# Kernel tuning notes

Hardware: AMD Instinct MI355X
Metric: run time of the kernel (lower is better)

The kernel has to match this reference:

```python
import jax, jax.numpy as jnp
import numpy as np

B, L, D, FF = 4, 4096, 1024, 4096
EPS = 1e-06


def setup_inputs() -> dict:
    key = jax.random.key(0)
    ks = jax.random.split(key, 20)
    s_d = 1.0 / np.sqrt(D)
    s_ff = 1.0 / np.sqrt(FF)
    inp = {
        "x": jax.random.normal(ks[0], (B, L, D), jnp.float32),
        "hidden": jax.random.normal(ks[1], (B, D), jnp.float32),
        # sioconv linears (stored as [in, out])
        "w_ln_z": jax.random.normal(ks[2], (D, D), jnp.float32) * s_d,
        "b_ln_z": jnp.zeros((D,), jnp.float32),
        "w_dt": jax.random.normal(ks[3], (D, D), jnp.float32) * s_d,
        "b_dt": jnp.zeros((D,), jnp.float32),
        "w_y": jax.random.normal(ks[4], (D, D), jnp.float32) * s_d,
        "b_y": jnp.zeros((D,), jnp.float32),
        "w_y_act": jax.random.normal(ks[5], (D, D), jnp.float32) * s_d,
        "b_y_act": jnp.zeros((D,), jnp.float32),
        # FFN SwiGLU
        "w_fc": jax.random.normal(ks[6], (D, FF), jnp.float32) * s_d,
        "b_fc": jnp.zeros((FF,), jnp.float32),
        "w_fc_act": jax.random.normal(ks[7], (D, FF), jnp.float32) * s_d,
        "b_fc_act": jnp.zeros((FF,), jnp.float32),
        "w_out": jax.random.normal(ks[8], (FF, D), jnp.float32) * s_ff,
        "b_out": jnp.zeros((D,), jnp.float32),
        # RMSNorm gains
        "g_sio": jnp.ones((D,), jnp.float32),
        "g_ffn": jnp.ones((D,), jnp.float32),
    }
    return inp


def _rmsnorm(x, g):
    return x * jax.lax.rsqrt(jnp.mean(x * x, axis=-1, keepdims=True) + EPS) * g


def _sioconv(x, hidden, w_ln_z, b_ln_z, w_dt, b_dt, w_y, b_y, w_y_act, b_y_act):
    # x: [B,L,D], hidden: [B,D]
    ln_z = -jax.nn.softplus(-(x @ w_ln_z + b_ln_z))       # [B,L,D]
    dt = x @ w_dt + b_dt
    ln_da = -jax.nn.softplus(-dt)
    ln_o_da = -jax.nn.softplus(dt)
    ln_o_da_cumsum = jnp.cumsum(ln_o_da, axis=1)
    # inner-chunk: exp(logcumsumexp(ln_z + ln_da - cumsum) + cumsum)
    lse = jax.lax.cumlogsumexp(ln_z + ln_da - ln_o_da_cumsum, axis=1)
    h_inner = jnp.exp(lse + ln_o_da_cumsum)
    # cross-chunk: decay applied to incoming hidden state
    h_cross = jnp.exp(ln_o_da_cumsum) * hidden[:, None, :]
    h = h_inner + h_cross
    y = (h @ w_y + b_y) * jax.nn.silu(x @ w_y_act + b_y_act)
    return y, h


def _ffn(x, w_fc, b_fc, w_fc_act, b_fc_act, w_out, b_out):
    return (x @ w_fc + b_fc) * jax.nn.silu(x @ w_fc_act + b_fc_act) @ w_out + b_out


def reference(x, hidden, w_ln_z, b_ln_z, w_dt, b_dt, w_y, b_y, w_y_act, b_y_act,
              w_fc, b_fc, w_fc_act, b_fc_act, w_out, b_out, g_sio, g_ffn):
    x_res = x
    y, h = _sioconv(_rmsnorm(x, g_sio), hidden,
                    w_ln_z, b_ln_z, w_dt, b_dt, w_y, b_y, w_y_act, b_y_act)
    x = y + x_res  # dropout is identity (p=0 / eval)
    x_res = x
    x = _ffn(_rmsnorm(x, g_ffn), w_fc, b_fc, w_fc_act, b_fc_act, w_out, b_out) + x_res
    return (x, h)
```

## Files before the change

kernel.cpp:

```cpp
#include <hip/hip_runtime.h>
#include <stdint.h>

using u16 = unsigned short;
typedef __attribute__((ext_vector_type(8))) __bf16 bf16x8;
typedef __attribute__((ext_vector_type(4))) float f32x4;

#define DEV __device__ __forceinline__

static constexpr int kB = 4, kL = 4096, kD = 1024, kFF = 4096;
static constexpr int kM = kB * kL;
static constexpr int kLC = 256, kNC = kL / kLC;
static constexpr float kEPS = 1e-6f;

DEV u16 f2bf(float v) {
  union { float f; uint32_t u; } x; x.f = v;
  uint32_t r = x.u + 0x7FFFu + ((x.u >> 16) & 1u);
  return (u16)(r >> 16);
}
DEV float bf2f(u16 u) {
  union { uint32_t u; float f; } x; x.u = (uint32_t)u << 16; return x.f;
}
DEV float sigm(float x) { return 1.0f / (1.0f + __expf(-x)); }

DEV void gload_lds16(const void* g, void* l) {
  __builtin_amdgcn_global_load_lds(
      (const __attribute__((address_space(1))) void*)g,
      (__attribute__((address_space(3))) void*)l, 16, 0, 0);
}

__global__ __launch_bounds__(256) void wtrans_kernel(const float* __restrict__ in,
                                                     u16* __restrict__ out,
                                                     int K, int N) {
  __shared__ float t[32][33];
  const int n0 = blockIdx.x * 32, k0 = blockIdx.y * 32;
  const int tx = threadIdx.x, ty = threadIdx.y;
#pragma unroll
  for (int i = 0; i < 4; ++i)
    t[ty + i * 8][tx] = in[(size_t)(k0 + ty + i * 8) * N + (n0 + tx)];
  __syncthreads();
#pragma unroll
  for (int i = 0; i < 4; ++i)
    out[(size_t)(n0 + ty + i * 8) * K + (k0 + tx)] = f2bf(t[tx][ty + i * 8]);
}

__global__ __launch_bounds__(256) void wtrans_pair(const float* __restrict__ a,
                                                   const float* __restrict__ b,
                                                   u16* __restrict__ out,
                                                   int K, int Ncols) {
  __shared__ float t[32][33];
  const int n0 = blockIdx.x * 32, k0 = blockIdx.y * 32;
  const int sel = (n0 >> 5) & 1;
  const int c0 = (n0 >> 6) * 32;
  const float* __restrict__ src = sel ? b : a;
  const int tx = threadIdx.x, ty = threadIdx.y;
#pragma unroll
  for (int i = 0; i < 4; ++i)
    t[ty + i * 8][tx] = src[(size_t)(k0 + ty + i * 8) * Ncols + (c0 + tx)];
  __syncthreads();
#pragma unroll
  for (int i = 0; i < 4; ++i)
    out[(size_t)(n0 + ty + i * 8) * K + (k0 + tx)] = f2bf(t[tx][ty + i * 8]);
}

__global__ __launch_bounds__(256) void rmsnorm_kernel(const float* __restrict__ x,
                                                      const float* __restrict__ g,
                                                      u16* __restrict__ out) {
  const int row = blockIdx.x;
  const int t = threadIdx.x;
  const float4 v = ((const float4*)(x + (size_t)row * kD))[t];
  float ss = v.x * v.x + v.y * v.y + v.z * v.z + v.w * v.w;
#pragma unroll
  for (int o = 1; o < 64; o <<= 1) ss += __shfl_xor(ss, o, 64);
  __shared__ float red[4];
  if ((t & 63) == 0) red[t >> 6] = ss;
  __syncthreads();
  const float tot = red[0] + red[1] + red[2] + red[3];
  const float sc = rsqrtf(tot * (1.0f / kD) + kEPS);
  const float4 gv = ((const float4*)g)[t];
  const uint32_t lo = (uint32_t)f2bf(v.x * sc * gv.x) | ((uint32_t)f2bf(v.y * sc * gv.y) << 16);
  const uint32_t hi = (uint32_t)f2bf(v.z * sc * gv.z) | ((uint32_t)f2bf(v.w * sc * gv.w) << 16);
  *(uint2*)(out + (size_t)row * kD + t * 4) = make_uint2(lo, hi);
}

template <int MODE>
__global__ __launch_bounds__(512) void gemm256(
    const u16* __restrict__ A, const u16* __restrict__ Bt,
    const float* __restrict__ bias, const float* __restrict__ bias2,
    const u16* __restrict__ aux, int auxld,
    const float* __restrict__ res, float* __restrict__ Cf,
    u16* __restrict__ Cb, float* __restrict__ C2,
    int M, int N, int K) {
  __shared__ u16 sm[65536];
  const int tid = threadIdx.x;
  const int lane = tid & 63;
  const int wave = tid >> 6;
  const int wr = wave >> 2, wc = wave & 3;

  const int gx = gridDim.x;
  const int nwg = gx * gridDim.y;
  const int bid = blockIdx.y * gx + blockIdx.x;
  const int q = nwg >> 3, r = nwg & 7;
  const int xcd = bid & 7, idx0 = bid >> 3;
  const int wg = (xcd < r ? xcd * (q + 1) : r * (q + 1) + (xcd - r) * q) + idx0;
  const int m0 = (wg / gx) * 256, n0 = (wg % gx) * 256;

  const int NK = K >> 6;

  const int l8 = lane >> 3, l7 = lane & 7;
  const int rsub = wave * 8 + l8;
  const int kel = (l7 ^ l8) * 8;
  const size_t srcA = (size_t)(m0 + rsub) * K + kel;
  const size_t srcB = (size_t)(n0 + rsub) * K + kel;

  auto stage_half = [&](int kt, int half) {
    const int bsel = (kt & 1) * 32768;
    if (half < 2) {
      u16* d = sm + bsel + tid * 8 + half * 8192;
      const u16* s = A + srcA + (size_t)kt * 64 + (size_t)(half * 2) * 64 * K;
      gload_lds16(s, d);
      gload_lds16(s + (size_t)64 * K, d + 4096);
    } else {
      const int hh = half - 2;
      u16* d = sm + bsel + 16384 + tid * 8 + hh * 8192;
      const u16* s = Bt + srcB + (size_t)kt * 64 + (size_t)(hh * 2) * 64 * K;
      gload_lds16(s, d);
      gload_lds16(s + (size_t)64 * K, d + 4096);
    }
  };

  const int ra = lane & 15;
  const int kx0 = ((lane >> 4) ^ l7) * 8;
  const int kx1 = (((lane >> 4) + 4) ^ l7) * 8;

  f32x4 acc[8][4] = {};
  bf16x8 al[4][2], ah[4][2], bl[2][2], bh[2][2];

  stage_half(0, 0); stage_half(0, 1); stage_half(0, 2); stage_half(0, 3);
  stage_half(1, 0);
  asm volatile("s_waitcnt vmcnt(2)");
  asm volatile("s_barrier" ::: "memory");

  for (int h = 0; h < NK; ++h) {
    const u16* Az = sm + (h & 1) * 32768 + (wr * 128 + ra) * 64;
    const u16* Bz = sm + (h & 1) * 32768 + 16384 + (wc * 64 + ra) * 64;

#pragma unroll
    for (int mi = 0; mi < 4; ++mi) {
      al[mi][0] = *(const bf16x8*)(Az + mi * 16 * 64 + kx0);
      al[mi][1] = *(const bf16x8*)(Az + mi * 16 * 64 + kx1);
    }
#pragma unroll
    for (int ni = 0; ni < 2; ++ni) {
      bl[ni][0] = *(const bf16x8*)(Bz + ni * 16 * 64 + kx0);
      bl[ni][1] = *(const bf16x8*)(Bz + ni * 16 * 64 + kx1);
    }
    if (h + 1 < NK) stage_half(h + 1, 1);
    asm volatile("s_barrier" ::: "memory");
    asm volatile("s_waitcnt lgkmcnt(0)");
    __builtin_amdgcn_s_setprio(1);
#pragma unroll
    for (int mi = 0; mi < 4; ++mi)
#pragma unroll
      for (int ni = 0; ni < 2; ++ni)
#pragma unroll
        for (int kk = 0; kk < 2; ++kk)
          acc[mi][ni] = __builtin_amdgcn_mfma_f32_16x16x32_bf16(al[mi][kk], bl[ni][kk], acc[mi][ni], 0, 0, 0);
    __builtin_amdgcn_s_setprio(0);
    asm volatile("s_barrier" ::: "memory");

#pragma unroll
    for (int ni = 0; ni < 2; ++ni) {
      bh[ni][0] = *(const bf16x8*)(Bz + (32 + ni * 16) * 64 + kx0);
      bh[ni][1] = *(const bf16x8*)(Bz + (32 + ni * 16) * 64 + kx1);
    }
    if (h + 1 < NK) stage_half(h + 1, 2);
    asm volatile("s_barrier" ::: "memory");
    asm volatile("s_waitcnt lgkmcnt(0)");
    __builtin_amdgcn_s_setprio(1);
#pragma unroll
    for (int mi = 0; mi < 4; ++mi)
#pragma unroll
      for (int ni = 0; ni < 2; ++ni)
#pragma unroll
        for (int kk = 0; kk < 2; ++kk)
          acc[mi][2 + ni] = __builtin_amdgcn_mfma_f32_16x16x32_bf16(al[mi][kk], bh[ni][kk], acc[mi][2 + ni], 0, 0, 0);
    __builtin_amdgcn_s_setprio(0);
    asm volatile("s_barrier" ::: "memory");

#pragma unroll
    for (int mi = 0; mi < 4; ++mi) {
      ah[mi][0] = *(const bf16x8*)(Az + (64 + mi * 16) * 64 + kx0);
      ah[mi][1] = *(const bf16x8*)(Az + (64 + mi * 16) * 64 + kx1);
    }
    if (h + 1 < NK) stage_half(h + 1, 3);
    asm volatile("s_barrier" ::: "memory");
    asm volatile("s_waitcnt lgkmcnt(0)");
    __builtin_amdgcn_s_setprio(1);
#pragma unroll
    for (int mi = 0; mi < 4; ++mi)
#pragma unroll
      for (int ni = 0; ni < 2; ++ni)
#pragma unroll
        for (int kk = 0; kk < 2; ++kk)
          acc[4 + mi][ni] = __builtin_amdgcn_mfma_f32_16x16x32_bf16(ah[mi][kk], bl[ni][kk], acc[4 + mi][ni], 0, 0, 0);
    __builtin_amdgcn_s_setprio(0);
    asm volatile("s_barrier" ::: "memory");

    if (h + 2 < NK) stage_half(h + 2, 0);
    asm volatile("s_barrier" ::: "memory");
    __builtin_amdgcn_s_setprio(1);
#pragma unroll
    for (int mi = 0; mi < 4; ++mi)
#pragma unroll
      for (int ni = 0; ni < 2; ++ni)
#pragma unroll
        for (int kk = 0; kk < 2; ++kk)
          acc[4 + mi][2 + ni] = __builtin_amdgcn_mfma_f32_16x16x32_bf16(ah[mi][kk], bh[ni][kk], acc[4 + mi][2 + ni], 0, 0, 0);
    __builtin_amdgcn_s_setprio(0);
    if (h + 2 < NK) asm volatile("s_waitcnt vmcnt(2)");
    else            asm volatile("s_waitcnt vmcnt(0)");
    asm volatile("s_barrier" ::: "memory");
  }

  const int ca = ra;
  const int rq = (lane >> 4) * 4;
  if (MODE == 6 || MODE == 7) {
    const int Nout = N >> 1;
#pragma unroll
    for (int mi = 0; mi < 8; ++mi) {
#pragma unroll
      for (int ni = 0; ni < 2; ++ni) {
        const int cout = (n0 >> 1) + wc * 32 + ni * 16 + ca;
        const float b1 = bias[cout], b2 = bias2[cout];
#pragma unroll
        for (int j = 0; j < 4; ++j) {
          const int rr = m0 + wr * 128 + mi * 16 + rq + j;
          const size_t idx = (size_t)rr * Nout + cout;
          const float v1 = acc[mi][ni][j] + b1;
          const float v2 = acc[mi][2 + ni][j] + b2;
          if (MODE == 7) {
            Cf[idx] = sigm(-v2);
            C2[idx] = sigm(v1) * sigm(v2);
          } else {
            Cb[idx] = f2bf(v2 * (v1 * sigm(v1)));
          }
        }
      }
    }
  } else {
#pragma unroll
    for (int mi = 0; mi < 8; ++mi) {
#pragma unroll
      for (int ni = 0; ni < 4; ++ni) {
        const int c = n0 + wc * 64 + ni * 16 + ca;
        const float bz = bias[c];
#pragma unroll
        for (int j = 0; j < 4; ++j) {
          const int rr = m0 + wr * 128 + mi * 16 + rq + j;
          const size_t idx = (size_t)rr * N + c;
          const float v = acc[mi][ni][j] + bz;
          if (MODE == 2) {
            const float a = bf2f(aux[(size_t)rr * auxld + c]);
            Cf[idx] = v * (a * sigm(a)) + res[idx];
          } else if (MODE == 4) {
            Cf[idx] = v + res[idx];
          } else {
            Cb[idx] = f2bf(v);
          }
        }
      }
    }
  }
}

__global__ __launch_bounds__(256) void scan_phase1(const float* __restrict__ Aa,
                                                   const float* __restrict__ Bv,
                                                   float* __restrict__ P,
                                                   float* __restrict__ S) {
  const int d = blockIdx.x * 256 + threadIdx.x;
  const int c = blockIdx.y, b = blockIdx.z;
  size_t base = ((size_t)b * kL + (size_t)c * kLC) * kD + d;
  float p = 1.0f, s = 0.0f;
#pragma unroll 4
  for (int l = 0; l < kLC; ++l) {
    const float a = Aa[base];
    const float bv = Bv[base];
    p *= a;
    s = fmaf(a, s, bv);
    base += kD;
  }
  const size_t o = ((size_t)b * kNC + c) * kD + d;
  P[o] = p; S[o] = s;
}

__global__ __launch_bounds__(256) void scan_phase2(const float* __restrict__ P,
                                                   const float* __restrict__ S,
                                                   const float* __restrict__ hidden,
                                                   float* __restrict__ Hini) {
  const int d = blockIdx.x * 256 + threadIdx.x;
  const int b = blockIdx.y;
  float carry = hidden[(size_t)b * kD + d];
  for (int c = 0; c < kNC; ++c) {
    const size_t o = ((size_t)b * kNC + c) * kD + d;
    Hini[o] = carry;
    carry = fmaf(P[o], carry, S[o]);
  }
}

__global__ __launch_bounds__(256) void scan_phase3(const float* __restrict__ Aa,
                                                   const float* __restrict__ Bv,
                                                   const float* __restrict__ Hini,
                                                   float* __restrict__ Hout,
                                                   u16* __restrict__ Hbf) {
  const int d = blockIdx.x * 256 + threadIdx.x;
  const int c = blockIdx.y, b = blockIdx.z;
  float h = Hini[((size_t)b * kNC + c) * kD + d];
  size_t base = ((size_t)b * kL + (size_t)c * kLC) * kD + d;
#pragma unroll 4
  for (int l = 0; l < kLC; ++l) {
    h = fmaf(Aa[base], h, Bv[base]);
    Hout[base] = h;
    Hbf[base] = f2bf(h);
    base += kD;
  }
}

extern "C" void kernel_launch(void* const* d_in, const int* in_sizes, int n_in,
                              void* d_out, int out_size, void* d_ws, size_t ws_size,
                              hipStream_t stream) {
  const float* x      = (const float*)d_in[0];
  const float* hidden = (const float*)d_in[1];
  const float* w_ln_z = (const float*)d_in[2];
  const float* b_ln_z = (const float*)d_in[3];
  const float* w_dt   = (const float*)d_in[4];
  const float* b_dt   = (const float*)d_in[5];
  const float* w_y    = (const float*)d_in[6];
  const float* b_y    = (const float*)d_in[7];
  const float* w_yact = (const float*)d_in[8];
  const float* b_yact = (const float*)d_in[9];
  const float* w_fc   = (const float*)d_in[10];
  const float* b_fc   = (const float*)d_in[11];
  const float* w_fca  = (const float*)d_in[12];
  const float* b_fca  = (const float*)d_in[13];
  const float* w_out  = (const float*)d_in[14];
  const float* b_out  = (const float*)d_in[15];
  const float* g_sio  = (const float*)d_in[16];
  const float* g_ffn  = (const float*)d_in[17];

  char* ws = (char*)d_ws;
  const size_t MiB = 1ull << 20;
  u16* wzdT  = (u16*)(ws + 0 * MiB);
  u16* wyaT  = (u16*)(ws + 4 * MiB);
  u16* wyT   = (u16*)(ws + 6 * MiB);
  u16* wfgT  = (u16*)(ws + 8 * MiB);
  u16* woutT = (u16*)(ws + 24 * MiB);
  u16*   xn    = (u16*)(ws + 33 * MiB);
  u16*   yabuf = (u16*)(ws + 65 * MiB);
  float* Abuf  = (float*)(ws + 97 * MiB);
  float* Bvbuf = (float*)(ws + 161 * MiB);
  u16*   hbf   = (u16*)(ws + 225 * MiB);
  u16*   Ubuf  = (u16*)(ws + 161 * MiB);
  float* Pbuf  = (float*)(ws + 289 * MiB);
  float* Sbuf  = (float*)(ws + 290 * MiB);
  float* Hini  = (float*)(ws + 291 * MiB);

  float* xout = (float*)d_out;
  float* hout = xout + (size_t)kM * kD;
  float* x1 = Abuf;

  const dim3 tb(32, 8);
  wtrans_pair<<<dim3(2048 / 32, kD / 32), tb, 0, stream>>>(w_ln_z, w_dt, wzdT, kD, kD);
  wtrans_pair<<<dim3(8192 / 32, kD / 32), tb, 0, stream>>>(w_fca, w_fc, wfgT, kD, kFF);
  wtrans_kernel<<<dim3(kD / 32, kD / 32), tb, 0, stream>>>(w_yact, wyaT, kD, kD);
  wtrans_kernel<<<dim3(kD / 32, kD / 32), tb, 0, stream>>>(w_y, wyT, kD, kD);
  wtrans_kernel<<<dim3(kD / 32, kFF / 32), tb, 0, stream>>>(w_out, woutT, kFF, kD);

  rmsnorm_kernel<<<kM, 256, 0, stream>>>(x, g_sio, xn);

  gemm256<7><<<dim3(2048 / 256, kM / 256), 512, 0, stream>>>(
      xn, wzdT, b_ln_z, b_dt, nullptr, 0, nullptr, Abuf, nullptr, Bvbuf, kM, 2048, kD);
  gemm256<5><<<dim3(kD / 256, kM / 256), 512, 0, stream>>>(
      xn, wyaT, b_yact, nullptr, nullptr, 0, nullptr, nullptr, yabuf, nullptr, kM, kD, kD);

  scan_phase1<<<dim3(kD / 256, kNC, kB), 256, 0, stream>>>(Abuf, Bvbuf, Pbuf, Sbuf);
  scan_phase2<<<dim3(kD / 256, kB), 256, 0, stream>>>(Pbuf, Sbuf, hidden, Hini);
  scan_phase3<<<dim3(kD / 256, kNC, kB), 256, 0, stream>>>(Abuf, Bvbuf, Hini, hout, hbf);

  gemm256<2><<<dim3(kD / 256, kM / 256), 512, 0, stream>>>(
      hbf, wyT, b_y, nullptr, yabuf, kD, x, x1, nullptr, nullptr, kM, kD, kD);

  rmsnorm_kernel<<<kM, 256, 0, stream>>>(x1, g_ffn, xn);

  gemm256<6><<<dim3(8192 / 256, kM / 256), 512, 0, stream>>>(
      xn, wfgT, b_fca, b_fc, nullptr, 0, nullptr, nullptr, Ubuf, nullptr, kM, 8192, kD);

  gemm256<4><<<dim3(kD / 256, kM / 256), 512, 0, stream>>>(
      Ubuf, woutT, b_out, nullptr, nullptr, 0, x1, xout, nullptr, nullptr, kM, kD, kFF);
}
```

Before: 767.5 us.

## Add dedicated 256x128 SwiGLU FFN GEMM and merge weight transposes

Replaces the 256x256-tile gemm256<6> for the FFN gate/up projection with a new gemm_ffn kernel. The new kernel uses 256x128 tiles with K=32 stages, a smaller LDS footprint, launch_bounds(512,4) for higher occupancy, and an XCD-aware workgroup remap for L2 locality. It also fuses the five weight-transpose launches into one wtrans_all kernel to cut launch overhead. The trade-off is that smaller tiles lower arithmetic intensity per block, in exchange for more concurrent waves and better latency hiding.

```diff
diff --git a/kernel.cpp b/kernel.cpp
--- a/kernel.cpp
+++ b/kernel.cpp
@@ -28,31 +28,26 @@
       (__attribute__((address_space(3))) void*)l, 16, 0, 0);
 }
 
-__global__ __launch_bounds__(256) void wtrans_kernel(const float* __restrict__ in,
-                                                     u16* __restrict__ out,
-                                                     int K, int N) {
+__global__ __launch_bounds__(256) void wtrans_all(
+    const float* __restrict__ w_ln_z, const float* __restrict__ w_dt,
+    const float* __restrict__ w_fca, const float* __restrict__ w_fc,
+    const float* __restrict__ w_yact, const float* __restrict__ w_y,
+    const float* __restrict__ w_out_,
+    u16* __restrict__ wzdT, u16* __restrict__ wfgT, u16* __restrict__ wyaT,
+    u16* __restrict__ wyT, u16* __restrict__ woutT) {
+  const int bid = blockIdx.x;
+  const float *a, *b; u16* out; int K, Ncols, bx, local; bool pair;
+  if (bid < 2048)       { local = bid;         a = w_ln_z; b = w_dt; out = wzdT;  K = 1024; Ncols = 1024; bx = 64;  pair = true;  }
+  else if (bid < 10240) { local = bid - 2048;  a = w_fca;  b = w_fc; out = wfgT;  K = 1024; Ncols = 4096; bx = 256; pair = true;  }
+  else if (bid < 11264) { local = bid - 10240; a = w_yact; b = nullptr; out = wyaT; K = 1024; Ncols = 1024; bx = 32; pair = false; }
+  else if (bid < 12288) { local = bid - 11264; a = w_y;    b = nullptr; out = wyT;  K = 1024; Ncols = 1024; bx = 32; pair = false; }
+  else                  { local = bid - 12288; a = w_out_; b = nullptr; out = woutT; K = 4096; Ncols = 1024; bx = 32; pair = false; }
+  const int n0 = (local % bx) * 32, k0 = (local / bx) * 32;
   __shared__ float t[32][33];
-  const int n0 = blockIdx.x * 32, k0 = blockIdx.y * 32;
   const int tx = threadIdx.x, ty = threadIdx.y;
-#pragma unroll
-  for (int i = 0; i < 4; ++i)
-    t[ty + i * 8][tx] = in[(size_t)(k0 + ty + i * 8) * N + (n0 + tx)];
-  __syncthreads();
-#pragma unroll
-  for (int i = 0; i < 4; ++i)
-    out[(size_t)(n0 + ty + i * 8) * K + (k0 + tx)] = f2bf(t[tx][ty + i * 8]);
-}
-
-__global__ __launch_bounds__(256) void wtrans_pair(const float* __restrict__ a,
-                                                   const float* __restrict__ b,
-                                                   u16* __restrict__ out,
-                                                   int K, int Ncols) {
-  __shared__ float t[32][33];
-  const int n0 = blockIdx.x * 32, k0 = blockIdx.y * 32;
-  const int sel = (n0 >> 5) & 1;
-  const int c0 = (n0 >> 6) * 32;
-  const float* __restrict__ src = sel ? b : a;
-  const int tx = threadIdx.x, ty = threadIdx.y;
+  const float* src; int c0;
+  if (pair) { src = ((n0 >> 5) & 1) ? b : a; c0 = (n0 >> 6) * 32; }
+  else      { src = a; c0 = n0; }
 #pragma unroll
   for (int i = 0; i < 4; ++i)
     t[ty + i * 8][tx] = src[(size_t)(k0 + ty + i * 8) * Ncols + (c0 + tx)];
@@ -141,18 +136,18 @@
   asm volatile("s_barrier" ::: "memory");
 
   for (int h = 0; h < NK; ++h) {
-    const u16* Az = sm + (h & 1) * 32768 + (wr * 128 + ra) * 64;
-    const u16* Bz = sm + (h & 1) * 32768 + 16384 + (wc * 64 + ra) * 64;
+    const u16* as = sm + (h & 1) * 32768 + (wr * 128 + ra) * 64;
+    const u16* bs = sm + (h & 1) * 32768 + 16384 + (wc * 64 + ra) * 64;
 
 #pragma unroll
     for (int mi = 0; mi < 4; ++mi) {
-      al[mi][0] = *(const bf16x8*)(Az + mi * 16 * 64 + kx0);
-      al[mi][1] = *(const bf16x8*)(Az + mi * 16 * 64 + kx1);
+      al[mi][0] = *(const bf16x8*)(as + mi * 16 * 64 + kx0);
+      al[mi][1] = *(const bf16x8*)(as + mi * 16 * 64 + kx1);
     }
 #pragma unroll
     for (int ni = 0; ni < 2; ++ni) {
-      bl[ni][0] = *(const bf16x8*)(Bz + ni * 16 * 64 + kx0);
-      bl[ni][1] = *(const bf16x8*)(Bz + ni * 16 * 64 + kx1);
+      bl[ni][0] = *(const bf16x8*)(bs + ni * 16 * 64 + kx0);
+      bl[ni][1] = *(const bf16x8*)(bs + ni * 16 * 64 + kx1);
     }
     if (h + 1 < NK) stage_half(h + 1, 1);
     asm volatile("s_barrier" ::: "memory");
@@ -170,8 +165,8 @@
 
 #pragma unroll
     for (int ni = 0; ni < 2; ++ni) {
-      bh[ni][0] = *(const bf16x8*)(Bz + (32 + ni * 16) * 64 + kx0);
-      bh[ni][1] = *(const bf16x8*)(Bz + (32 + ni * 16) * 64 + kx1);
+      bh[ni][0] = *(const bf16x8*)(bs + (32 + ni * 16) * 64 + kx0);
+      bh[ni][1] = *(const bf16x8*)(bs + (32 + ni * 16) * 64 + kx1);
     }
     if (h + 1 < NK) stage_half(h + 1, 2);
     asm volatile("s_barrier" ::: "memory");
@@ -189,8 +184,8 @@
 
 #pragma unroll
     for (int mi = 0; mi < 4; ++mi) {
-      ah[mi][0] = *(const bf16x8*)(Az + (64 + mi * 16) * 64 + kx0);
-      ah[mi][1] = *(const bf16x8*)(Az + (64 + mi * 16) * 64 + kx1);
+      ah[mi][0] = *(const bf16x8*)(as + (64 + mi * 16) * 64 + kx0);
+      ah[mi][1] = *(const bf16x8*)(as + (64 + mi * 16) * 64 + kx1);
     }
     if (h + 1 < NK) stage_half(h + 1, 3);
     asm volatile("s_barrier" ::: "memory");
@@ -224,7 +219,7 @@
 
   const int ca = ra;
   const int rq = (lane >> 4) * 4;
-  if (MODE == 6 || MODE == 7) {
+  if (MODE == 7) {
     const int Nout = N >> 1;
 #pragma unroll
     for (int mi = 0; mi < 8; ++mi) {
@@ -238,12 +233,8 @@
           const size_t idx = (size_t)rr * Nout + cout;
           const float v1 = acc[mi][ni][j] + b1;
           const float v2 = acc[mi][2 + ni][j] + b2;
-          if (MODE == 7) {
-            Cf[idx] = sigm(-v2);
-            C2[idx] = sigm(v1) * sigm(v2);
-          } else {
-            Cb[idx] = f2bf(v2 * (v1 * sigm(v1)));
-          }
+          Cf[idx] = sigm(-v2);
+          C2[idx] = sigm(v1) * sigm(v2);
         }
       }
     }
@@ -268,6 +259,119 @@
             Cb[idx] = f2bf(v);
           }
         }
+      }
+    }
+  }
+}
+
+__global__ __launch_bounds__(512, 4) void gemm_ffn(
+    const u16* __restrict__ A, const u16* __restrict__ Bt,
+    const float* __restrict__ bias, const float* __restrict__ bias2,
+    u16* __restrict__ Cb, int M, int N, int K) {
+  __shared__ u16 sm[24576];
+  const int tid = threadIdx.x;
+  const int lane = tid & 63;
+  const int wave = tid >> 6;
+  const int wr = wave >> 1, wc = wave & 1;
+
+  const int gx = gridDim.x;
+  const int nwg = gx * gridDim.y;
+  const int bid = blockIdx.y * gx + blockIdx.x;
+  const int q = nwg >> 3, r = nwg & 7;
+  const int xcd = bid & 7, idx0 = bid >> 3;
+  const int wg = (xcd < r ? xcd * (q + 1) : r * (q + 1) + (xcd - r) * q) + idx0;
+  const int per = gridDim.y * 4;
+  const int sg = wg / per, srem = wg % per;
+  const int m0 = (srem >> 2) * 256;
+  const int n0 = (sg * 4 + (srem & 3)) * 128;
+
+  const int NK = K >> 5;
+
+  const int rsub = wave * 16 + (lane >> 2);
+  const int kel = ((lane & 3) ^ ((lane >> 3) & 3)) * 8;
+  const size_t srcA = (size_t)(m0 + rsub) * K + kel;
+  const size_t srcB = (size_t)(n0 + rsub) * K + kel;
+
+  auto stageA = [&](int kt) {
+    u16* d = sm + (kt & 1) * 12288 + tid * 8;
+    const u16* s = A + srcA + (size_t)kt * 32;
+    gload_lds16(s, d);
+    gload_lds16(s + (size_t)128 * K, d + 4096);
+  };
+  auto stageB = [&](int kt) {
+    gload_lds16(Bt + srcB + (size_t)kt * 32,
+                sm + (kt & 1) * 12288 + 8192 + tid * 8);
+  };
+
+  const int ra = lane & 15;
+  const int rb = ra * 32 + ((((lane >> 4) ^ (ra >> 1)) & 3) << 3);
+
+  f32x4 acc[4][4] = {};
+  bf16x8 af[4], bfr[4];
+
+  stageA(0); stageB(0);
+  if (NK > 1) { stageA(1); stageB(1); }
+  asm volatile("s_waitcnt vmcnt(3)");
+  asm volatile("s_barrier" ::: "memory");
+
+  for (int h = 0; h < NK; ++h) {
+    const u16* Az = sm + (h & 1) * 12288 + wr * 2048;
+    const u16* Bz = sm + (h & 1) * 12288 + 8192 + wc * 2048;
+
+#pragma unroll
+    for (int mi = 0; mi < 4; ++mi) af[mi] = *(const bf16x8*)(Az + mi * 512 + rb);
+    bfr[0] = *(const bf16x8*)(Bz + rb);
+    bfr[1] = *(const bf16x8*)(Bz + 512 + rb);
+    asm volatile("s_barrier" ::: "memory");
+    asm volatile("s_waitcnt lgkmcnt(0)");
+    __builtin_amdgcn_s_setprio(1);
+#pragma unroll
+    for (int mi = 0; mi < 4; ++mi)
+#pragma unroll
+      for (int ni = 0; ni < 2; ++ni)
+        acc[mi][ni] = __builtin_amdgcn_mfma_f32_16x16x32_bf16(af[mi], bfr[ni], acc[mi][ni], 0, 0, 0);
+    __builtin_amdgcn_s_setprio(0);
+    asm volatile("s_barrier" ::: "memory");
+
+    bfr[2] = *(const bf16x8*)(Bz + 1024 + rb);
+    bfr[3] = *(const bf16x8*)(Bz + 1536 + rb);
+    if (h + 2 < NK) stageA(h + 2);
+    asm volatile("s_barrier" ::: "memory");
+    asm volatile("s_waitcnt lgkmcnt(0)");
+    __builtin_amdgcn_s_setprio(1);
+#pragma unroll
+    for (int mi = 0; mi < 4; ++mi)
+      acc[mi][2] = __builtin_amdgcn_mfma_f32_16x16x32_bf16(af[mi], bfr[2], acc[mi][2], 0, 0, 0);
+    __builtin_amdgcn_s_setprio(0);
+    asm volatile("s_barrier" ::: "memory");
+
+    if (h + 2 < NK) stageB(h + 2);
+    __builtin_amdgcn_s_setprio(1);
+#pragma unroll
+    for (int mi = 0; mi < 4; ++mi)
+      acc[mi][3] = __builtin_amdgcn_mfma_f32_16x16x32_bf16(af[mi], bfr[3], acc[mi][3], 0, 0, 0);
+    __builtin_amdgcn_s_setprio(0);
+    if (h + 2 < NK) asm volatile("s_waitcnt vmcnt(3)");
+    else            asm volatile("s_waitcnt vmcnt(0)");
+    asm volatile("s_barrier" ::: "memory");
+  }
+
+  const int ca = lane & 15;
+  const int rq = (lane >> 4) * 4;
+  const int Nout = N >> 1;
+#pragma unroll
+  for (int mi = 0; mi < 4; ++mi) {
+#pragma unroll
+    for (int ni = 0; ni < 2; ++ni) {
+      const int cout = (n0 >> 1) + wc * 32 + ni * 16 + ca;
+      const float b1 = bias[cout], b2 = bias2[cout];
+#pragma unroll
+      for (int j = 0; j < 4; ++j) {
+        const int rr = m0 + wr * 64 + mi * 16 + rq + j;
+        const size_t idx = (size_t)rr * Nout + cout;
+        const float v1 = acc[mi][ni][j] + b1;
+        const float v2 = acc[mi][2 + ni][j] + b2;
+        Cb[idx] = f2bf(v2 * (v1 * sigm(v1)));
       }
     }
   }
@@ -368,12 +472,9 @@
   float* hout = xout + (size_t)kM * kD;
   float* x1 = Abuf;
 
-  const dim3 tb(32, 8);
-  wtrans_pair<<<dim3(2048 / 32, kD / 32), tb, 0, stream>>>(w_ln_z, w_dt, wzdT, kD, kD);
-  wtrans_pair<<<dim3(8192 / 32, kD / 32), tb, 0, stream>>>(w_fca, w_fc, wfgT, kD, kFF);
-  wtrans_kernel<<<dim3(kD / 32, kD / 32), tb, 0, stream>>>(w_yact, wyaT, kD, kD);
-  wtrans_kernel<<<dim3(kD / 32, kD / 32), tb, 0, stream>>>(w_y, wyT, kD, kD);
-  wtrans_kernel<<<dim3(kD / 32, kFF / 32), tb, 0, stream>>>(w_out, woutT, kFF, kD);
+  wtrans_all<<<16384, dim3(32, 8), 0, stream>>>(
+      w_ln_z, w_dt, w_fca, w_fc, w_yact, w_y, w_out,
+      wzdT, wfgT, wyaT, wyT, woutT);
 
   rmsnorm_kernel<<<kM, 256, 0, stream>>>(x, g_sio, xn);
 
@@ -391,8 +492,8 @@
 
   rmsnorm_kernel<<<kM, 256, 0, stream>>>(x1, g_ffn, xn);
 
-  gemm256<6><<<dim3(8192 / 256, kM / 256), 512, 0, stream>>>(
-      xn, wfgT, b_fca, b_fc, nullptr, 0, nullptr, nullptr, Ubuf, nullptr, kM, 8192, kD);
+  gemm_ffn<<<dim3(8192 / 128, kM / 256), 512, 0, stream>>>(
+      xn, wfgT, b_fca, b_fc, Ubuf, kM, 8192, kD);
 
   gemm256<4><<<dim3(kD / 256, kM / 256), 512, 0, stream>>>(
       Ubuf, woutT, b_out, nullptr, nullptr, 0, x1, xout, nullptr, nullptr, kM, kD, kFF);
```

New measurement: 759.1 us. About the same (-1.1%).
